# Kernel optimization log

Measured on AMD Instinct MI355X. Metric: run time of the kernel, lower is better.

Reference implementation:

```python
import jax, jax.numpy as jnp
import numpy as np

N_NODES = 100000
N_EDGES = 1600000
N_GRAPHS = 512
IN_DIM = 128
HID = 128
N_CLASSES = 10


def _gcn_conv(x, W, b, src, dst, n):
    """PyG GCNConv: out = D^{-1/2} (A+I) D^{-1/2} (x @ W) + b."""
    xw = x @ W  # [n, out_dim]
    loop = jnp.arange(n)
    s = jnp.concatenate([src, loop])  # add self loops
    d = jnp.concatenate([dst, loop])
    deg = jax.ops.segment_sum(jnp.ones(s.shape, dtype=xw.dtype), d, num_segments=n)
    dinv = jnp.where(deg > 0, jax.lax.rsqrt(deg), jnp.zeros((), xw.dtype))
    norm = dinv[s] * dinv[d]  # [E + n]
    out = jax.ops.segment_sum(xw[s] * norm[:, None], d, num_segments=n)
    return out + b


def _global_mean_pool(x, batch, num_graphs):
    sums = jax.ops.segment_sum(x, batch, num_segments=num_graphs)
    cnts = jax.ops.segment_sum(jnp.ones(batch.shape, dtype=x.dtype), batch, num_segments=num_graphs)
    return sums / jnp.maximum(cnts, 1.0)[:, None]


def setup_inputs() -> dict:
    key = jax.random.key(0)
    ks = jax.random.split(key, 8)
    x = jax.random.normal(ks[0], (N_NODES, IN_DIM), dtype=jnp.float32)
    edge_index = jax.random.randint(ks[1], (2, N_EDGES), 0, N_NODES, dtype=jnp.int64)
    batch = jnp.sort(jax.random.randint(ks[2], (N_NODES,), 0, N_GRAPHS, dtype=jnp.int64))
    sc = 1.0 / np.sqrt(IN_DIM)
    W1 = jax.random.normal(ks[3], (IN_DIM, HID), dtype=jnp.float32) * sc
    b1 = jnp.zeros((HID,), dtype=jnp.float32)
    W2 = jax.random.normal(ks[4], (HID, HID), dtype=jnp.float32) * (1.0 / np.sqrt(HID))
    b2 = jnp.zeros((HID,), dtype=jnp.float32)
    Wc = jax.random.normal(ks[5], (HID, N_CLASSES), dtype=jnp.float32) * (1.0 / np.sqrt(HID))
    bc = jnp.zeros((N_CLASSES,), dtype=jnp.float32)
    return {"x": x, "edge_index": edge_index, "batch": batch,
            "W1": W1, "b1": b1, "W2": W2, "b2": b2, "Wc": Wc, "bc": bc}


def reference(x, edge_index, batch, W1, b1, W2, b2, Wc, bc):
    src, dst = edge_index[0], edge_index[1]
    n = x.shape[0]
    h = _gcn_conv(x, W1, b1, src, dst, n)
    h = jax.nn.relu(h)
    h = _gcn_conv(h, W2, b2, src, dst, n)
    g = _global_mean_pool(h, batch, N_GRAPHS)
    return g @ Wc + bc
```

## Files before the change

kernel.cpp:

```cpp
#include <hip/hip_runtime.h>

#define N_NODES 100000
#define N_EDGES 1600000
#define N_GRAPHS 512
#define DIM 128
#define NCLS 10
#define NBKT 782
#define BCAP 2560

typedef __attribute__((ext_vector_type(8))) short short8;
typedef __attribute__((ext_vector_type(4))) float f32x4;

static __device__ __forceinline__ unsigned short f2bf(float f) {
    unsigned u = __float_as_uint(f);
    unsigned r = (u + 0x7FFF + ((u >> 16) & 1)) >> 16;
    return (unsigned short)r;
}
static __device__ __forceinline__ float bf2f(unsigned u) {
    return __uint_as_float(u << 16);
}


__global__ void k_wprep(const float* __restrict__ W1, const float* __restrict__ W2,
                        unsigned short* __restrict__ wf1, unsigned short* __restrict__ wf2,
                        int* __restrict__ bcnt) {
    int b = blockIdx.x;
    if (b >= 128) {
        int i = (b - 128) * 256 + threadIdx.x;
        if (i < NBKT) bcnt[i] = 0;
        return;
    }
    const float* W = (b < 64) ? W1 : W2;
    unsigned short* wfrag = (b < 64) ? wf1 : wf2;
    int t = (b & 63) * 256 + threadIdx.x;
    int j = t & 7, lane = (t >> 3) & 63, nt = (t >> 9) & 7, kit = t >> 12;
    int k = kit * 32 + (lane >> 4) * 8 + j;
    int n = nt * 16 + (lane & 15);
    float v = W[k * 128 + n];
    unsigned short h = f2bf(v);
    wfrag[t] = h;
    wfrag[16384 + t] = f2bf(v - bf2f(h));
}


__global__ __launch_bounds__(256) void k_bucket(
    const int* __restrict__ src, const int* __restrict__ dst,
    int* __restrict__ bcnt, unsigned* __restrict__ bpack, int E) {
    __shared__ int cnt[NBKT];
    __shared__ int base[NBKT];
    int tid = threadIdx.x;
    for (int i = tid; i < NBKT; i += 256) cnt[i] = 0;
    __syncthreads();
    int e0 = blockIdx.x * 4096 + tid;
    unsigned pk[16]; short bk[16];
#pragma unroll
    for (int j = 0; j < 16; j++) {
        int e = e0 + j * 256;
        if (e < E) {
            int s = src[e], d = dst[e];
            bk[j] = (short)(d >> 7);
            pk[j] = ((unsigned)(d & 127) << 17) | (unsigned)s;
            atomicAdd(&cnt[bk[j]], 1);
        } else bk[j] = -1;
    }
    __syncthreads();
    for (int i = tid; i < NBKT; i += 256) {
        int c = cnt[i];
        base[i] = c ? atomicAdd(&bcnt[i], c) : 0;
        cnt[i] = 0;
    }
    __syncthreads();
#pragma unroll
    for (int j = 0; j < 16; j++) {
        if (bk[j] >= 0) {
            int p = base[bk[j]] + atomicAdd(&cnt[bk[j]], 1);
            if (p < BCAP) bpack[(size_t)bk[j] * BCAP + p] = pk[j];
        }
    }
}


static __device__ __forceinline__ void bsort_body(
    char* smemraw, int b,
    const unsigned* __restrict__ bpack, const int* __restrict__ bcnt,
    int* __restrict__ rp, float* __restrict__ dinv,
    int* __restrict__ esrc, int N, float* __restrict__ dvs) {
    int* lds      = (int*)smemraw;
    int* cnt      = lds + 256;
    int* scan     = lds + 384;
    int* cur      = lds + 512;
    int* gbase_sh = lds + 640;
    int tid = threadIdx.x;
    int v[4], pre[4];
    int s = 0;
#pragma unroll
    for (int j = 0; j < 4; j++) {
        int idx = tid * 4 + j;
        v[j] = (idx < NBKT) ? min(bcnt[idx], BCAP) : 0;
        pre[j] = s; s += v[j];
    }
    lds[tid] = s;
    __syncthreads();
    for (int off = 1; off < 256; off <<= 1) {
        int t = (tid >= off) ? lds[tid - off] : 0;
        __syncthreads();
        lds[tid] += t;
        __syncthreads();
    }
    if (tid == (b >> 2)) *gbase_sh = lds[tid] - s + pre[b & 3];
    if (tid < 128) cnt[tid] = 0;
    __syncthreads();
    int gbase = *gbase_sh;
    int n0 = b << 7;
    int m = min(bcnt[b], BCAP);
    const unsigned* bp = bpack + (size_t)b * BCAP;
    for (int j = tid; j < m; j += 256) atomicAdd(&cnt[bp[j] >> 17], 1);
    __syncthreads();
    if (tid < 128) scan[tid] = cnt[tid];
    __syncthreads();
    for (int off = 1; off < 128; off <<= 1) {
        int t = (tid < 128 && tid >= off) ? scan[tid - off] : 0;
        __syncthreads();
        if (tid < 128) scan[tid] += t;
        __syncthreads();
    }
    if (tid < 128) {
        int c = cnt[tid];
        int excl = scan[tid] - c;
        int node = n0 + tid;
        float dv = rsqrtf((float)(c + 1));
        if (node <= N) rp[node] = gbase + excl;
        if (node < N) dinv[node] = dv;
        dvs[tid] = dv;
        cur[tid] = gbase + excl;
    }
    __syncthreads();
    for (int j = tid; j < m; j += 256) {
        unsigned pk = bp[j];
        int p = atomicAdd(&cur[pk >> 17], 1);
        esrc[p] = (int)(pk & 0x1FFFF);
    }
}

static __device__ __forceinline__ void gemm_f32_body(
    char* smemraw, int rowBlk,
    const float* __restrict__ A, const unsigned short* __restrict__ wfrag,
    const float* __restrict__ dvs, unsigned short* __restrict__ ybf, int M) {
    unsigned short* ldsw = (unsigned short*)smemraw;
    int tid = threadIdx.x, wave = tid >> 6, lane = tid & 63;
    int m = lane & 15, quad = lane >> 4;
    int rowBase = rowBlk * 128 + wave * 32;
    int r0 = rowBase + m, r1 = rowBase + 16 + m;
    for (int i = tid; i < 2048; i += 256)
        ((short8*)ldsw)[i] = ((const short8*)wfrag)[i];
    __syncthreads();
    f32x4 acc0[8], acc1[8];
#pragma unroll
    for (int i = 0; i < 8; i++) { acc0[i] = (f32x4){0,0,0,0}; acc1[i] = (f32x4){0,0,0,0}; }
    const unsigned short* wlo = wfrag + 16384;

#pragma unroll
    for (int kit = 0; kit < 4; kit++) {
        float a0[8], a1[8];
        if (r0 < M) {
            const float4* ap = (const float4*)(A + (size_t)r0 * 128 + kit * 32 + quad * 8);
            float4 f0 = ap[0], f1 = ap[1];
            a0[0]=f0.x; a0[1]=f0.y; a0[2]=f0.z; a0[3]=f0.w; a0[4]=f1.x; a0[5]=f1.y; a0[6]=f1.z; a0[7]=f1.w;
        } else { for (int j = 0; j < 8; j++) a0[j] = 0.f; }
        if (r1 < M) {
            const float4* ap = (const float4*)(A + (size_t)r1 * 128 + kit * 32 + quad * 8);
            float4 f0 = ap[0], f1 = ap[1];
            a1[0]=f0.x; a1[1]=f0.y; a1[2]=f0.z; a1[3]=f0.w; a1[4]=f1.x; a1[5]=f1.y; a1[6]=f1.z; a1[7]=f1.w;
        } else { for (int j = 0; j < 8; j++) a1[j] = 0.f; }
        short8 ahi0, alo0, ahi1, alo1;
#pragma unroll
        for (int j = 0; j < 8; j++) {
            unsigned short h0 = f2bf(a0[j]);
            ahi0[j] = (short)h0; alo0[j] = (short)f2bf(a0[j] - bf2f(h0));
            unsigned short h1 = f2bf(a1[j]);
            ahi1[j] = (short)h1; alo1[j] = (short)f2bf(a1[j] - bf2f(h1));
        }
        int fb = kit * 4096 + lane * 8;
#pragma unroll
        for (int nt = 0; nt < 8; nt++) {
            int idx = fb + nt * 512;
            short8 bhi = *(const short8*)(ldsw + idx);
            short8 blo = *(const short8*)(wlo + idx);
            acc0[nt] = __builtin_amdgcn_mfma_f32_16x16x32_bf16(ahi0, bhi, acc0[nt], 0, 0, 0);
            acc0[nt] = __builtin_amdgcn_mfma_f32_16x16x32_bf16(alo0, bhi, acc0[nt], 0, 0, 0);
            acc0[nt] = __builtin_amdgcn_mfma_f32_16x16x32_bf16(ahi0, blo, acc0[nt], 0, 0, 0);
            acc1[nt] = __builtin_amdgcn_mfma_f32_16x16x32_bf16(ahi1, bhi, acc1[nt], 0, 0, 0);
            acc1[nt] = __builtin_amdgcn_mfma_f32_16x16x32_bf16(alo1, bhi, acc1[nt], 0, 0, 0);
            acc1[nt] = __builtin_amdgcn_mfma_f32_16x16x32_bf16(ahi1, blo, acc1[nt], 0, 0, 0);
        }
    }
    __syncthreads();
    unsigned short* wsm = ldsw + wave * 32 * 136;
#pragma unroll
    for (int rg = 0; rg < 4; rg++) {
        float s0 = dvs[wave * 32 + quad * 4 + rg];
        float s1 = dvs[wave * 32 + 16 + quad * 4 + rg];
#pragma unroll
        for (int nt = 0; nt < 8; nt++) {
            wsm[(quad * 4 + rg) * 136 + nt * 16 + m] = f2bf(acc0[nt][rg] * s0);
            wsm[(16 + quad * 4 + rg) * 136 + nt * 16 + m] = f2bf(acc1[nt][rg] * s1);
        }
    }
    __syncthreads();
#pragma unroll
    for (int i = 0; i < 8; i++) {
        int rl = i * 4 + quad;
        int grow = rowBase + rl;
        if (grow < M) {
            short8 v = *(const short8*)(wsm + rl * 136 + m * 8);
            *(short8*)(ybf + (size_t)grow * 128 + m * 8) = v;
        }
    }
}


__global__ __launch_bounds__(256) void k_fuse(
    const unsigned* __restrict__ bpack, const int* __restrict__ bcnt,
    int* __restrict__ rp, float* __restrict__ dinv, int* __restrict__ esrc, int N,
    const float* __restrict__ A, const unsigned short* __restrict__ wfrag,
    unsigned short* __restrict__ ybf, int M) {
    __shared__ __align__(16) char smem[4 * 32 * 136 * 2];
    __shared__ float dvs[128];
    int b = blockIdx.x;
    bsort_body(smem, b, bpack, bcnt, rp, dinv, esrc, N, dvs);
    __syncthreads();
    gemm_f32_body(smem, b, A, wfrag, dvs, ybf, M);
}


__global__ __launch_bounds__(256) void k_aggemm2(
    const unsigned short* __restrict__ y, const float* __restrict__ dinv,
    const int* __restrict__ rp, const int* __restrict__ esrc,
    const float* __restrict__ bias, const unsigned short* __restrict__ wfrag,
    unsigned short* __restrict__ ybf, int N) {
    __shared__ unsigned h1[32 * 68];
    int tid = threadIdx.x, wave = tid >> 6, lane = tid & 63;
    int slab = blockIdx.x * 32;
    const unsigned* y2 = (const unsigned*)y;
    float2 bv = ((const float2*)bias)[lane];

    for (int ni = 0; ni < 8; ni++) {
        int lr = wave * 8 + ni;
        int node = slab + lr;
        unsigned packed = 0;
        if (node < N) {
            unsigned vs = y2[(size_t)node * 64 + lane];
            float a0 = bf2f(vs & 0xFFFF), a1 = bf2f(vs >> 16);
            int beg = rp[node], end = rp[node + 1];
            int j = beg;
            while (j < end) {
                int idxv = (j + lane < end) ? esrc[j + lane] : 0;
                int cnt = end - j; if (cnt > 64) cnt = 64;
                int i = 0;
                for (; i + 4 <= cnt; i += 4) {
                    int s0 = __shfl(idxv, i + 0);
                    int s1 = __shfl(idxv, i + 1);
                    int s2 = __shfl(idxv, i + 2);
                    int s3 = __shfl(idxv, i + 3);
                    unsigned v0 = y2[(size_t)s0 * 64 + lane];
                    unsigned v1 = y2[(size_t)s1 * 64 + lane];
                    unsigned v2 = y2[(size_t)s2 * 64 + lane];
                    unsigned v3 = y2[(size_t)s3 * 64 + lane];
                    a0 += bf2f(v0 & 0xFFFF); a1 += bf2f(v0 >> 16);
                    a0 += bf2f(v1 & 0xFFFF); a1 += bf2f(v1 >> 16);
                    a0 += bf2f(v2 & 0xFFFF); a1 += bf2f(v2 >> 16);
                    a0 += bf2f(v3 & 0xFFFF); a1 += bf2f(v3 >> 16);
                }
                for (; i < cnt; i++) {
                    int s = __shfl(idxv, i);
                    unsigned v = y2[(size_t)s * 64 + lane];
                    a0 += bf2f(v & 0xFFFF); a1 += bf2f(v >> 16);
                }
                j += cnt;
            }
            float s = dinv[node];
            float o0 = fmaxf(s * a0 + bv.x, 0.f);
            float o1 = fmaxf(s * a1 + bv.y, 0.f);
            packed = (unsigned)f2bf(o0) | ((unsigned)f2bf(o1) << 16);
        }
        h1[lr * 68 + lane] = packed;
    }
    __syncthreads();

    const unsigned short* h1us = (const unsigned short*)h1;
    int m = lane & 15, quad = lane >> 4;
    f32x4 acc0[2], acc1[2];
#pragma unroll
    for (int i = 0; i < 2; i++) { acc0[i] = (f32x4){0,0,0,0}; acc1[i] = (f32x4){0,0,0,0}; }
    const unsigned short* wlo = wfrag + 16384;
#pragma unroll
    for (int kit = 0; kit < 4; kit++) {
        short8 ah0 = *(const short8*)(h1us + m * 136 + kit * 32 + quad * 8);
        short8 ah1 = *(const short8*)(h1us + (16 + m) * 136 + kit * 32 + quad * 8);
#pragma unroll
        for (int ct = 0; ct < 2; ct++) {
            int idx = kit * 4096 + lane * 8 + (wave * 2 + ct) * 512;
            short8 bhi = *(const short8*)(wfrag + idx);
            short8 blo = *(const short8*)(wlo + idx);
            acc0[ct] = __builtin_amdgcn_mfma_f32_16x16x32_bf16(ah0, bhi, acc0[ct], 0, 0, 0);
            acc0[ct] = __builtin_amdgcn_mfma_f32_16x16x32_bf16(ah0, blo, acc0[ct], 0, 0, 0);
            acc1[ct] = __builtin_amdgcn_mfma_f32_16x16x32_bf16(ah1, bhi, acc1[ct], 0, 0, 0);
            acc1[ct] = __builtin_amdgcn_mfma_f32_16x16x32_bf16(ah1, blo, acc1[ct], 0, 0, 0);
        }
    }
    float dv0 = (slab + m < N) ? dinv[slab + m] : 0.f;
    float dv1 = (slab + 16 + m < N) ? dinv[slab + 16 + m] : 0.f;
    __syncthreads();
    unsigned short* wsm = (unsigned short*)h1;
#pragma unroll
    for (int rg = 0; rg < 4; rg++) {
        float s0 = __shfl(dv0, quad * 4 + rg);
        float s1 = __shfl(dv1, quad * 4 + rg);
#pragma unroll
        for (int ct = 0; ct < 2; ct++) {
            int colb = (wave * 2 + ct) * 16 + m;
            wsm[(quad * 4 + rg) * 136 + colb] = f2bf(acc0[ct][rg] * s0);
            wsm[(16 + quad * 4 + rg) * 136 + colb] = f2bf(acc1[ct][rg] * s1);
        }
    }
    __syncthreads();
#pragma unroll
    for (int pass = 0; pass < 2; pass++) {
        int flat = pass * 256 + tid;
        int rl = flat >> 4, c8 = flat & 15;
        int grow = slab + rl;
        if (grow < N) {
            short8 v = *(const short8*)(wsm + rl * 136 + c8 * 8);
            *(short8*)(ybf + (size_t)grow * 128 + c8 * 8) = v;
        }
    }
}


__global__ __launch_bounds__(256) void k_agg(
    const unsigned short* __restrict__ y, const float* __restrict__ dinv,
    const int* __restrict__ rp, const int* __restrict__ esrc,
    const float* __restrict__ bias, unsigned* __restrict__ out, int relu, int N) {
    int wave = threadIdx.x >> 6;
    int lane = threadIdx.x & 63;
    int node = blockIdx.x * 4 + wave;
    if (node >= N) return;
    const unsigned* y2 = (const unsigned*)y;
    unsigned vs = y2[(size_t)node * 64 + lane];
    float a0 = bf2f(vs & 0xFFFF), a1 = bf2f(vs >> 16);
    int beg = rp[node], end = rp[node + 1];
    int j = beg;
    while (j < end) {
        int idxv = (j + lane < end) ? esrc[j + lane] : 0;
        int cnt = end - j; if (cnt > 64) cnt = 64;
        int i = 0;
        for (; i + 4 <= cnt; i += 4) {
            int s0 = __shfl(idxv, i + 0);
            int s1 = __shfl(idxv, i + 1);
            int s2 = __shfl(idxv, i + 2);
            int s3 = __shfl(idxv, i + 3);
            unsigned v0 = y2[(size_t)s0 * 64 + lane];
            unsigned v1 = y2[(size_t)s1 * 64 + lane];
            unsigned v2 = y2[(size_t)s2 * 64 + lane];
            unsigned v3 = y2[(size_t)s3 * 64 + lane];
            a0 += bf2f(v0 & 0xFFFF); a1 += bf2f(v0 >> 16);
            a0 += bf2f(v1 & 0xFFFF); a1 += bf2f(v1 >> 16);
            a0 += bf2f(v2 & 0xFFFF); a1 += bf2f(v2 >> 16);
            a0 += bf2f(v3 & 0xFFFF); a1 += bf2f(v3 >> 16);
        }
        for (; i < cnt; i++) {
            int s = __shfl(idxv, i);
            unsigned v = y2[(size_t)s * 64 + lane];
            a0 += bf2f(v & 0xFFFF); a1 += bf2f(v >> 16);
        }
        j += cnt;
    }
    float s = dinv[node];
    float2 bv = ((const float2*)bias)[lane];
    float o0 = s * a0 + bv.x;
    float o1 = s * a1 + bv.y;
    if (relu) { o0 = fmaxf(o0, 0.f); o1 = fmaxf(o1, 0.f); }
    out[(size_t)node * 64 + lane] = (unsigned)f2bf(o0) | ((unsigned)f2bf(o1) << 16);
}


__global__ __launch_bounds__(256) void k_poolhead(
    const unsigned* __restrict__ h2, const int* __restrict__ batch,
    const float* __restrict__ Wc, const float* __restrict__ bc,
    float* __restrict__ out, int n) {
    __shared__ float2 red[4][64];
    __shared__ float grow[DIM];
    int gid = blockIdx.x;
    int tid = threadIdx.x, wave = tid >> 6, lane = tid & 63;
    int lo = 0, hi = n;
    while (lo < hi) { int mid = (lo + hi) >> 1; if (batch[mid] < gid) lo = mid + 1; else hi = mid; }
    int start = lo;
    hi = n;
    while (lo < hi) { int mid = (lo + hi) >> 1; if (batch[mid] < gid + 1) lo = mid + 1; else hi = mid; }
    int end = lo;
    float a0 = 0.f, a1 = 0.f;
    for (int r = start + wave; r < end; r += 4) {
        unsigned v = h2[(size_t)r * 64 + lane];
        a0 += bf2f(v & 0xFFFF); a1 += bf2f(v >> 16);
    }
    red[wave][lane] = make_float2(a0, a1);
    __syncthreads();
    if (tid < 64) {
        float2 s = red[0][tid];
        s.x += red[1][tid].x; s.y += red[1][tid].y;
        s.x += red[2][tid].x; s.y += red[2][tid].y;
        s.x += red[3][tid].x; s.y += red[3][tid].y;
        int cnt = end - start;
        float inv = 1.f / (float)(cnt > 0 ? cnt : 1);
        grow[tid * 2] = s.x * inv;
        grow[tid * 2 + 1] = s.y * inv;
    }
    __syncthreads();
    if (tid < NCLS) {
        float acc = bc[tid];
#pragma unroll 16
        for (int k = 0; k < DIM; k++) acc += grow[k] * Wc[k * NCLS + tid];
        out[gid * NCLS + tid] = acc;
    }
}

extern "C" void kernel_launch(void* const* d_in, const int* in_sizes, int n_in,
                              void* d_out, int out_size, void* d_ws, size_t ws_size,
                              hipStream_t stream) {
    const float* x    = (const float*)d_in[0];
    const int*   ei   = (const int*)d_in[1];
    const int*   batch= (const int*)d_in[2];
    const float* W1   = (const float*)d_in[3];
    const float* b1   = (const float*)d_in[4];
    const float* W2   = (const float*)d_in[5];
    const float* b2   = (const float*)d_in[6];
    const float* Wc   = (const float*)d_in[7];
    const float* bc   = (const float*)d_in[8];
    float* out = (float*)d_out;
    const int N = N_NODES, E = N_EDGES;
    const int* src = ei;
    const int* dst = ei + E;

    char* ws = (char*)d_ws;
    size_t off = 0;
    auto carve = [&](size_t bytes) -> void* {
        void* p = ws + off;
        off = (off + bytes + 255) & ~(size_t)255;
        return p;
    };
    int*      rp    = (int*)     carve((size_t)(N + 1) * 4);
    float*    dinv  = (float*)   carve((size_t)N * 4);
    int*      bcnt  = (int*)     carve(NBKT * 4);
    unsigned* bpack = (unsigned*)carve((size_t)NBKT * BCAP * 4);
    int*      esrc  = (int*)     carve((size_t)E * 4);
    unsigned short* wf1 = (unsigned short*)carve(2 * 16384 * 2);
    unsigned short* wf2 = (unsigned short*)carve(2 * 16384 * 2);
    unsigned short* bufY = (unsigned short*)carve((size_t)N * DIM * 2);
    unsigned short* bufH = (unsigned short*)carve((size_t)N * DIM * 2);
    (void)ws_size; (void)n_in; (void)in_sizes; (void)out_size;

    const int nbBkt = (E + 4095) / 4096;

    hipLaunchKernelGGL(k_wprep,  dim3(128 + (NBKT + 255) / 256), dim3(256), 0, stream, W1, W2, wf1, wf2, bcnt);
    hipLaunchKernelGGL(k_bucket, dim3(nbBkt), dim3(256), 0, stream, src, dst, bcnt, bpack, E);
    hipLaunchKernelGGL(k_fuse, dim3(NBKT), dim3(256), 0, stream,
                       bpack, bcnt, rp, dinv, esrc, N, x, wf1, bufY, N);
    hipLaunchKernelGGL(k_aggemm2, dim3((N + 31) / 32), dim3(256), 0, stream,
                       bufY, dinv, rp, esrc, b1, wf2, bufH, N);
    hipLaunchKernelGGL(k_agg, dim3((N + 3) / 4), dim3(256), 0, stream, bufH, dinv, rp, esrc, b2, (unsigned*)bufY, 0, N);
    hipLaunchKernelGGL(k_poolhead, dim3(N_GRAPHS), dim3(256), 0, stream, (const unsigned*)bufY, batch, Wc, bc, out, N);
}
```

Baseline: 325.3 us.

## Fuse second aggregation with classifier projection and atomic mean-pool accumulation

The final GCN aggregation now projects each node's 128-dim output directly through the classifier weights using wave reductions. It then atomically adds the 10-class partials into per-graph accumulators instead of writing the hidden features to memory. A tiny final kernel divides by node counts and adds the bias, and the pool/head kernel's re-read of all node features is removed. This relies on linearity of mean-pool and the head, and it adds per-block atomics and non-deterministic float summation order.

Result: slower. 400.2 us (+23.1%).

```diff
diff --git a/kernel.cpp b/kernel.cpp
--- a/kernel.cpp
+++ b/kernel.cpp
@@ -23,11 +23,15 @@
 
 __global__ void k_wprep(const float* __restrict__ W1, const float* __restrict__ W2,
                         unsigned short* __restrict__ wf1, unsigned short* __restrict__ wf2,
-                        int* __restrict__ bcnt) {
+                        int* __restrict__ bcnt, float* __restrict__ acc) {
     int b = blockIdx.x;
     if (b >= 128) {
-        int i = (b - 128) * 256 + threadIdx.x;
-        if (i < NBKT) bcnt[i] = 0;
+        if (b < 132) {
+            int i = (b - 128) * 256 + threadIdx.x;
+            if (i < NBKT) bcnt[i] = 0;
+        } else {
+            for (int i = threadIdx.x; i < N_GRAPHS * NCLS; i += 256) acc[i] = 0.f;
+        }
         return;
     }
     const float* W = (b < 64) ? W1 : W2;
@@ -337,91 +341,93 @@
 }
 
 
-__global__ __launch_bounds__(256) void k_agg(
+__global__ __launch_bounds__(256) void k_aggpool(
     const unsigned short* __restrict__ y, const float* __restrict__ dinv,
     const int* __restrict__ rp, const int* __restrict__ esrc,
-    const float* __restrict__ bias, unsigned* __restrict__ out, int relu, int N) {
+    const float* __restrict__ bias, const float* __restrict__ Wc,
+    const int* __restrict__ batch, float* __restrict__ acc, int N) {
+    __shared__ float red[4][NCLS];
+    __shared__ int gsh[4];
     int wave = threadIdx.x >> 6;
     int lane = threadIdx.x & 63;
     int node = blockIdx.x * 4 + wave;
-    if (node >= N) return;
-    const unsigned* y2 = (const unsigned*)y;
-    unsigned vs = y2[(size_t)node * 64 + lane];
-    float a0 = bf2f(vs & 0xFFFF), a1 = bf2f(vs >> 16);
-    int beg = rp[node], end = rp[node + 1];
-    int j = beg;
-    while (j < end) {
-        int idxv = (j + lane < end) ? esrc[j + lane] : 0;
-        int cnt = end - j; if (cnt > 64) cnt = 64;
-        int i = 0;
-        for (; i + 4 <= cnt; i += 4) {
-            int s0 = __shfl(idxv, i + 0);
-            int s1 = __shfl(idxv, i + 1);
-            int s2 = __shfl(idxv, i + 2);
-            int s3 = __shfl(idxv, i + 3);
-            unsigned v0 = y2[(size_t)s0 * 64 + lane];
-            unsigned v1 = y2[(size_t)s1 * 64 + lane];
-            unsigned v2 = y2[(size_t)s2 * 64 + lane];
-            unsigned v3 = y2[(size_t)s3 * 64 + lane];
-            a0 += bf2f(v0 & 0xFFFF); a1 += bf2f(v0 >> 16);
-            a0 += bf2f(v1 & 0xFFFF); a1 += bf2f(v1 >> 16);
-            a0 += bf2f(v2 & 0xFFFF); a1 += bf2f(v2 >> 16);
-            a0 += bf2f(v3 & 0xFFFF); a1 += bf2f(v3 >> 16);
-        }
-        for (; i < cnt; i++) {
-            int s = __shfl(idxv, i);
-            unsigned v = y2[(size_t)s * 64 + lane];
-            a0 += bf2f(v & 0xFFFF); a1 += bf2f(v >> 16);
-        }
-        j += cnt;
-    }
-    float s = dinv[node];
-    float2 bv = ((const float2*)bias)[lane];
-    float o0 = s * a0 + bv.x;
-    float o1 = s * a1 + bv.y;
-    if (relu) { o0 = fmaxf(o0, 0.f); o1 = fmaxf(o1, 0.f); }
-    out[(size_t)node * 64 + lane] = (unsigned)f2bf(o0) | ((unsigned)f2bf(o1) << 16);
-}
-
-
-__global__ __launch_bounds__(256) void k_poolhead(
-    const unsigned* __restrict__ h2, const int* __restrict__ batch,
-    const float* __restrict__ Wc, const float* __restrict__ bc,
-    float* __restrict__ out, int n) {
-    __shared__ float2 red[4][64];
-    __shared__ float grow[DIM];
-    int gid = blockIdx.x;
-    int tid = threadIdx.x, wave = tid >> 6, lane = tid & 63;
+    bool valid = node < N;
+    float o0 = 0.f, o1 = 0.f;
+    if (valid) {
+        const unsigned* y2 = (const unsigned*)y;
+        unsigned vs = y2[(size_t)node * 64 + lane];
+        float a0 = bf2f(vs & 0xFFFF), a1 = bf2f(vs >> 16);
+        int beg = rp[node], end = rp[node + 1];
+        int j = beg;
+        while (j < end) {
+            int idxv = (j + lane < end) ? esrc[j + lane] : 0;
+            int cnt = end - j; if (cnt > 64) cnt = 64;
+            int i = 0;
+            for (; i + 4 <= cnt; i += 4) {
+                int s0 = __shfl(idxv, i + 0);
+                int s1 = __shfl(idxv, i + 1);
+                int s2 = __shfl(idxv, i + 2);
+                int s3 = __shfl(idxv, i + 3);
+                unsigned v0 = y2[(size_t)s0 * 64 + lane];
+                unsigned v1 = y2[(size_t)s1 * 64 + lane];
+                unsigned v2 = y2[(size_t)s2 * 64 + lane];
+                unsigned v3 = y2[(size_t)s3 * 64 + lane];
+                a0 += bf2f(v0 & 0xFFFF); a1 += bf2f(v0 >> 16);
+                a0 += bf2f(v1 & 0xFFFF); a1 += bf2f(v1 >> 16);
+                a0 += bf2f(v2 & 0xFFFF); a1 += bf2f(v2 >> 16);
+                a0 += bf2f(v3 & 0xFFFF); a1 += bf2f(v3 >> 16);
+            }
+            for (; i < cnt; i++) {
+                int s = __shfl(idxv, i);
+                unsigned v = y2[(size_t)s * 64 + lane];
+                a0 += bf2f(v & 0xFFFF); a1 += bf2f(v >> 16);
+            }
+            j += cnt;
+        }
+        float s = dinv[node];
+        float2 bv = ((const float2*)bias)[lane];
+        o0 = s * a0 + bv.x;
+        o1 = s * a1 + bv.y;
+    }
+    if (lane == 0) gsh[wave] = valid ? batch[node] : -1;
+#pragma unroll
+    for (int c = 0; c < NCLS; c++) {
+        float p = o0 * Wc[(2 * lane) * NCLS + c] + o1 * Wc[(2 * lane + 1) * NCLS + c];
+        p += __shfl_xor(p, 1);  p += __shfl_xor(p, 2);  p += __shfl_xor(p, 4);
+        p += __shfl_xor(p, 8);  p += __shfl_xor(p, 16); p += __shfl_xor(p, 32);
+        if (lane == 0) red[wave][c] = p;
+    }
+    __syncthreads();
+    if (threadIdx.x < NCLS) {
+        int c = threadIdx.x;
+        int g0 = gsh[0], g3 = gsh[3];
+        if (g0 == g3 && g0 >= 0) {
+            atomicAdd(&acc[g0 * NCLS + c],
+                      red[0][c] + red[1][c] + red[2][c] + red[3][c]);
+        } else {
+#pragma unroll
+            for (int w = 0; w < 4; w++)
+                if (gsh[w] >= 0) atomicAdd(&acc[gsh[w] * NCLS + c], red[w][c]);
+        }
+    }
+}
+
+
+__global__ __launch_bounds__(256) void k_final(
+    const float* __restrict__ acc, const int* __restrict__ batch,
+    const float* __restrict__ bc, float* __restrict__ out, int n) {
+    int g = blockIdx.x * 256 + threadIdx.x;
+    if (g >= N_GRAPHS) return;
     int lo = 0, hi = n;
-    while (lo < hi) { int mid = (lo + hi) >> 1; if (batch[mid] < gid) lo = mid + 1; else hi = mid; }
+    while (lo < hi) { int mid = (lo + hi) >> 1; if (batch[mid] < g) lo = mid + 1; else hi = mid; }
     int start = lo;
     hi = n;
-    while (lo < hi) { int mid = (lo + hi) >> 1; if (batch[mid] < gid + 1) lo = mid + 1; else hi = mid; }
-    int end = lo;
-    float a0 = 0.f, a1 = 0.f;
-    for (int r = start + wave; r < end; r += 4) {
-        unsigned v = h2[(size_t)r * 64 + lane];
-        a0 += bf2f(v & 0xFFFF); a1 += bf2f(v >> 16);
-    }
-    red[wave][lane] = make_float2(a0, a1);
-    __syncthreads();
-    if (tid < 64) {
-        float2 s = red[0][tid];
-        s.x += red[1][tid].x; s.y += red[1][tid].y;
-        s.x += red[2][tid].x; s.y += red[2][tid].y;
-        s.x += red[3][tid].x; s.y += red[3][tid].y;
-        int cnt = end - start;
-        float inv = 1.f / (float)(cnt > 0 ? cnt : 1);
-        grow[tid * 2] = s.x * inv;
-        grow[tid * 2 + 1] = s.y * inv;
-    }
-    __syncthreads();
-    if (tid < NCLS) {
-        float acc = bc[tid];
-#pragma unroll 16
-        for (int k = 0; k < DIM; k++) acc += grow[k] * Wc[k * NCLS + tid];
-        out[gid * NCLS + tid] = acc;
-    }
+    while (lo < hi) { int mid = (lo + hi) >> 1; if (batch[mid] < g + 1) lo = mid + 1; else hi = mid; }
+    int cnt = lo - start;
+    float inv = 1.f / (float)(cnt > 0 ? cnt : 1);
+#pragma unroll
+    for (int c = 0; c < NCLS; c++)
+        out[g * NCLS + c] = acc[g * NCLS + c] * inv + bc[c];
 }
 
 extern "C" void kernel_launch(void* const* d_in, const int* in_sizes, int n_in,
@@ -455,18 +461,20 @@
     int*      esrc  = (int*)     carve((size_t)E * 4);
     unsigned short* wf1 = (unsigned short*)carve(2 * 16384 * 2);
     unsigned short* wf2 = (unsigned short*)carve(2 * 16384 * 2);
+    float*    gacc  = (float*)   carve((size_t)N_GRAPHS * NCLS * 4);
     unsigned short* bufY = (unsigned short*)carve((size_t)N * DIM * 2);
     unsigned short* bufH = (unsigned short*)carve((size_t)N * DIM * 2);
     (void)ws_size; (void)n_in; (void)in_sizes; (void)out_size;
 
     const int nbBkt = (E + 4095) / 4096;
 
-    hipLaunchKernelGGL(k_wprep,  dim3(128 + (NBKT + 255) / 256), dim3(256), 0, stream, W1, W2, wf1, wf2, bcnt);
+    hipLaunchKernelGGL(k_wprep,  dim3(133), dim3(256), 0, stream, W1, W2, wf1, wf2, bcnt, gacc);
     hipLaunchKernelGGL(k_bucket, dim3(nbBkt), dim3(256), 0, stream, src, dst, bcnt, bpack, E);
     hipLaunchKernelGGL(k_fuse, dim3(NBKT), dim3(256), 0, stream,
                        bpack, bcnt, rp, dinv, esrc, N, x, wf1, bufY, N);
     hipLaunchKernelGGL(k_aggemm2, dim3((N + 31) / 32), dim3(256), 0, stream,
                        bufY, dinv, rp, esrc, b1, wf2, bufH, N);
-    hipLaunchKernelGGL(k_agg, dim3((N + 3) / 4), dim3(256), 0, stream, bufH, dinv, rp, esrc, b2, (unsigned*)bufY, 0, N);
-    hipLaunchKernelGGL(k_poolhead, dim3(N_GRAPHS), dim3(256), 0, stream, (const unsigned*)bufY, batch, Wc, bc, out, N);
-}
+    hipLaunchKernelGGL(k_aggpool, dim3((N + 3) / 4), dim3(256), 0, stream,
+                       bufH, dinv, rp, esrc, b2, Wc, batch, gacc, N);
+    hipLaunchKernelGGL(k_final, dim3(2), dim3(256), 0, stream, gacc, batch, bc, out, N);
+}
```
